# Optimization experiments

Measured on AMD Instinct MI355X. Metric: run time of the kernel, lower is better.

Reference implementation:

```python
import jax, jax.numpy as jnp
import numpy as np

B, T, I, H, O = 32, 2048, 128, 512, 128
FORGET_BIAS = 1.0


def setup_inputs() -> dict:
    key = jax.random.key(0)
    ks = jax.random.split(key, 8)
    s_ih = 1.0 / np.sqrt(H)
    data = jax.random.normal(ks[0], (B, T, I), dtype=jnp.float32)
    h0 = jnp.zeros((B, H), dtype=jnp.float32)
    c0 = jnp.zeros((B, H), dtype=jnp.float32)
    W_ih = jax.random.uniform(ks[1], (4 * H, I), minval=-s_ih, maxval=s_ih, dtype=jnp.float32)
    W_hh = jax.random.uniform(ks[2], (4 * H, H), minval=-s_ih, maxval=s_ih, dtype=jnp.float32)
    b_ih = jax.random.uniform(ks[3], (4 * H,), minval=-s_ih, maxval=s_ih, dtype=jnp.float32)
    b_hh = jax.random.uniform(ks[4], (4 * H,), minval=-s_ih, maxval=s_ih, dtype=jnp.float32)
    # forget-gate bias init: slice [H:2H] of each bias filled with forget_bias/2
    b_ih = b_ih.at[H:2 * H].set(FORGET_BIAS / 2)
    b_hh = b_hh.at[H:2 * H].set(FORGET_BIAS / 2)
    lin_W = jax.random.uniform(ks[5], (O, H), minval=-s_ih, maxval=s_ih, dtype=jnp.float32)
    lin_b = jax.random.uniform(ks[6], (O,), minval=-s_ih, maxval=s_ih, dtype=jnp.float32)
    return dict(data=data, h0=h0, c0=c0, W_ih=W_ih, W_hh=W_hh,
                b_ih=b_ih, b_hh=b_hh, lin_W=lin_W, lin_b=lin_b)


def reference(data, h0, c0, W_ih, W_hh, b_ih, b_hh, lin_W, lin_b):
    # LSTMCell loop over time (batch_first). PyTorch gate order: i, f, g, o.
    # Original code appends the CELL state (variable `hidden` = c) to hs and
    # decodes from the stacked cell states — reproduced faithfully.
    bias = b_ih + b_hh  # [4H]

    def step(carry, x_t):
        h, c = carry
        gates = x_t @ W_ih.T + h @ W_hh.T + bias  # [B, 4H]
        i_g, f_g, g_g, o_g = jnp.split(gates, 4, axis=-1)
        c_new = jax.nn.sigmoid(f_g) * c + jax.nn.sigmoid(i_g) * jnp.tanh(g_g)
        h_new = jax.nn.sigmoid(o_g) * jnp.tanh(c_new)
        return (h_new, c_new), c_new

    xs = jnp.swapaxes(data, 0, 1)  # [T, B, I]
    (h_f, c_f), cs = jax.lax.scan(step, (h0, c0), xs)
    output = jnp.swapaxes(cs, 0, 1)  # [B, T, H]
    decoded = output @ lin_W.T + lin_b  # [B, T, O]
    return decoded, h_f, c_f
```

## Files before the change

### kernel.cpp

```cpp
#include <hip/hip_runtime.h>
#include <hip/hip_bf16.h>


#define B_ 32
#define T_ 2048
#define I_ 128
#define H_ 512
#define O_ 128
#define NG 8
#define BPG 4
#define WPG 32
#define NWG 256
#define NTHR 512

#define HXS 648
#define CPS 520

typedef short bf16x8 __attribute__((ext_vector_type(8)));
typedef float f32x4 __attribute__((ext_vector_type(4)));
typedef unsigned long long u64;

static __device__ __forceinline__ unsigned f2bf(float f) {
  unsigned u = __float_as_uint(f);
  u = u + 0x7FFFu + ((u >> 16) & 1u);
  return u >> 16;
}
static __device__ __forceinline__ float bf2f(unsigned h) {
  return __uint_as_float(h << 16);
}
static __device__ __forceinline__ float fsigm(float x) {
  return 1.0f / (1.0f + __expf(-x));
}
static __device__ __forceinline__ float ftanh(float x) {
  return 1.0f - 2.0f / (__expf(2.0f * x) + 1.0f);
}

#define ALD(p) __hip_atomic_load((p), __ATOMIC_RELAXED, __HIP_MEMORY_SCOPE_AGENT)
#define AST(p, v) __hip_atomic_store((p), (v), __ATOMIC_RELAXED, __HIP_MEMORY_SCOPE_AGENT)

__global__ __launch_bounds__(NTHR, 2) void lstm_fused(
    const float* __restrict__ data, const float* __restrict__ h0,
    const float* __restrict__ c0, const float* __restrict__ W_ih,
    const float* __restrict__ W_hh, const float* __restrict__ b_ih,
    const float* __restrict__ b_hh, const float* __restrict__ lin_W,
    const float* __restrict__ lin_b, float* __restrict__ out,
    float* __restrict__ ws) {
  __shared__ alignas(16) unsigned short sHxHi[BPG * HXS];
  __shared__ alignas(16) unsigned short sHxLo[BPG * HXS];
  __shared__ alignas(16) float sCprev[BPG * CPS];
  __shared__ alignas(16) float sLinW[4 * CPS];
  __shared__ alignas(16) float sGates[2 * 64 * 4];
  __shared__ alignas(16) float sCst[64];
  __shared__ alignas(16) float sBias[64];
  __shared__ float sLinB[4];

  const int bid = blockIdx.x;
  const int g = bid & 7;
  const int wgi = bid >> 3;
  const int b0 = g * BPG;
  const int ubase = wgi * 16;
  const int tid = threadIdx.x;
  const int lane = tid & 63;
  const int w = tid >> 6;
  const int gate = w >> 1;
  const int kh = w & 1;
  const int m16 = lane & 15;
  const int kcg = lane >> 4;

  float* cb = ws;
  unsigned* hbPk = (unsigned*)(ws + 32768);
  int* cnt = (int*)(ws + 65536);

  bf16x8 fAhi[10], fAlo[10];
  const int grow = gate * H_ + ubase + m16;
#pragma unroll
  for (int kk = 0; kk < 10; kk++) {
    int k = kh * 320 + kk * 32 + kcg * 8;
    const float* src = (k < H_) ? (W_hh + (size_t)grow * H_ + k)
                                : (W_ih + (size_t)grow * I_ + (k - H_));
    float4 v0 = *(const float4*)src;
    float4 v1 = *(const float4*)(src + 4);
    float w8[8] = {v0.x, v0.y, v0.z, v0.w, v1.x, v1.y, v1.z, v1.w};
    union { unsigned short u[8]; bf16x8 v; } hi, lo;
#pragma unroll
    for (int j = 0; j < 8; j++) {
      unsigned h = f2bf(w8[j]);
      hi.u[j] = (unsigned short)h;
      lo.u[j] = (unsigned short)f2bf(w8[j] - bf2f(h));
    }
    fAhi[kk] = hi.v;
    fAlo[kk] = lo.v;
  }
  if (tid < 64) {
    int u_ = tid >> 2, ga = tid & 3;
    int r = ga * H_ + ubase + u_;
    sBias[u_ * 4 + ga] = b_ih[r] + b_hh[r];
  }
  if (tid >= 64 && tid < 128) {
    int q = tid - 64;
    sCst[q] = c0[(size_t)(b0 + (q & 3)) * H_ + ubase + (q >> 2)];
  }
  for (int idx = tid; idx < 4 * H_; idx += NTHR) {
    int o = idx >> 9, k = idx & (H_ - 1);
    sLinW[o * CPS + k] = lin_W[(size_t)(wgi * 4 + o) * H_ + k];
  }
  if (tid < 4) sLinB[tid] = lin_b[wgi * 4 + tid];

  if (tid < 256) {
    int b = tid >> 6, off = (tid & 63) * 8;
    const float* src = h0 + (size_t)(b0 + b) * H_ + off;
    float4 v0 = *(const float4*)src;
    float4 v1 = *(const float4*)(src + 4);
    float w8[8] = {v0.x, v0.y, v0.z, v0.w, v1.x, v1.y, v1.z, v1.w};
    union { unsigned short u[8]; uint4 q; } hi, lo;
#pragma unroll
    for (int j = 0; j < 8; j++) {
      unsigned h = f2bf(w8[j]);
      hi.u[j] = (unsigned short)h;
      lo.u[j] = (unsigned short)f2bf(w8[j] - bf2f(h));
    }
    *(uint4*)&sHxHi[b * HXS + off] = hi.q;
    *(uint4*)&sHxLo[b * HXS + off] = lo.q;
  }
  if (tid >= 256 && tid < 384) {
    int i = tid - 256, b = i >> 5, c4 = i & 31;
    float4 v = *(const float4*)(data + ((size_t)(b0 + b) * T_) * I_ + c4 * 4);
    float w4[4] = {v.x, v.y, v.z, v.w};
    union { unsigned short u[4]; uint2 q; } hi, lo;
#pragma unroll
    for (int j = 0; j < 4; j++) {
      unsigned h = f2bf(w4[j]);
      hi.u[j] = (unsigned short)h;
      lo.u[j] = (unsigned short)f2bf(w4[j] - bf2f(h));
    }
    *(uint2*)&sHxHi[b * HXS + H_ + c4 * 4] = hi.q;
    *(uint2*)&sHxLo[b * HXS + H_ + c4 * 4] = lo.q;
  }
  float4 pfx;
  if (tid >= 320 && tid < 448) {
    int i = tid - 320, b = i >> 5, c4 = i & 31;
    int tp = (T_ > 1) ? 1 : 0;
    pfx = *(const float4*)(data + ((size_t)(b0 + b) * T_ + tp) * I_ + c4 * 4);
  }
  __syncthreads();

  const int bcl = (m16 < BPG) ? m16 : (BPG - 1);
  const unsigned short* pBhi = sHxHi + bcl * HXS + kh * 320 + kcg * 8;
  const unsigned short* pBlo = sHxLo + bcl * HXS + kh * 320 + kcg * 8;

  for (int t = 0; t < T_; t++) {
    f32x4 a0 = {0.f, 0.f, 0.f, 0.f}, a1 = a0, a2 = a0;
#pragma unroll
    for (int kk = 0; kk < 10; kk++) {
      bf16x8 bh = *(const bf16x8*)(pBhi + kk * 32);
      bf16x8 bl = *(const bf16x8*)(pBlo + kk * 32);
      a0 = __builtin_amdgcn_mfma_f32_16x16x32_bf16(fAhi[kk], bh, a0, 0, 0, 0);
      a1 = __builtin_amdgcn_mfma_f32_16x16x32_bf16(fAhi[kk], bl, a1, 0, 0, 0);
      a2 = __builtin_amdgcn_mfma_f32_16x16x32_bf16(fAlo[kk], bh, a2, 0, 0, 0);
    }
    if (m16 < BPG) {
#pragma unroll
      for (int j = 0; j < 4; j++) {
        int up = kcg * 4 + j;
        sGates[(kh * 64 + up * 4 + m16) * 4 + gate] = a0[j] + a1[j] + a2[j];
      }
    }
    __syncthreads();

    if (tid < 64) {
      int up = tid >> 2, b = tid & 3;
      const float4 p0 = *(const float4*)&sGates[(up * 4 + b) * 4];
      const float4 p1 = *(const float4*)&sGates[(64 + up * 4 + b) * 4];
      float gi = p0.x + p1.x + sBias[up * 4 + 0];
      float gf = p0.y + p1.y + sBias[up * 4 + 1];
      float gg = p0.z + p1.z + sBias[up * 4 + 2];
      float go = p0.w + p1.w + sBias[up * 4 + 3];
      float cn = fsigm(gf) * sCst[tid] + fsigm(gi) * ftanh(gg);
      float hn = fsigm(go) * ftanh(cn);
      sCst[tid] = cn;
      size_t sbase = (((size_t)(t & 1) * NG + g) * BPG + b) * H_ + ubase + up;
      AST(&cb[sbase], cn);
      unsigned hh = f2bf(hn);
      unsigned hl = f2bf(hn - bf2f(hh));
      AST(&hbPk[sbase], (hh << 16) | hl);
      if (t == T_ - 1) {
        const size_t DEC = (size_t)B_ * T_ * O_;
        out[DEC + (size_t)(b0 + b) * H_ + ubase + up] = hn;
        out[DEC + (size_t)B_ * H_ + (size_t)(b0 + b) * H_ + ubase + up] = cn;
      }
      asm volatile("s_waitcnt vmcnt(0)" ::: "memory");
      if (tid == 0)
        __hip_atomic_fetch_add(&cnt[g * 16], 1, __ATOMIC_RELAXED,
                               __HIP_MEMORY_SCOPE_AGENT);
      const int target = WPG * (t + 1);
      while (ALD(&cnt[g * 16]) < target) {}
    } else if (tid < 320) {
      if (t > 0) {
        int q = (tid >> 4) - 4;
        int ks = tid & 15;
        int o = q >> 2, b = q & 3;
        float s = 0.f;
#pragma unroll
        for (int j = 0; j < 32; j++) {
          int k = ks + j * 16;
          s += sLinW[o * CPS + k] * sCprev[b * CPS + k];
        }
        s += __shfl_xor(s, 1);
        s += __shfl_xor(s, 2);
        s += __shfl_xor(s, 4);
        s += __shfl_xor(s, 8);
        if (ks == 0)
          out[((size_t)(b0 + b) * T_ + (t - 1)) * O_ + wgi * 4 + o] =
              s + sLinB[o];
      }
    } else if (tid < 448) {
      int i = tid - 320, b = i >> 5, c4 = i & 31;
      union { unsigned short u[4]; uint2 q; } hi, lo;
      float w4[4] = {pfx.x, pfx.y, pfx.z, pfx.w};
#pragma unroll
      for (int j = 0; j < 4; j++) {
        unsigned h = f2bf(w4[j]);
        hi.u[j] = (unsigned short)h;
        lo.u[j] = (unsigned short)f2bf(w4[j] - bf2f(h));
      }
      *(uint2*)&sHxHi[b * HXS + H_ + c4 * 4] = hi.q;
      *(uint2*)&sHxLo[b * HXS + H_ + c4 * 4] = lo.q;
      int tp = (t + 2 < T_) ? t + 2 : T_ - 1;
      pfx = *(const float4*)(data + ((size_t)(b0 + b) * T_ + tp) * I_ + c4 * 4);
    }
    __syncthreads();

    {
      int b = tid >> 7, u4 = (tid & 127) * 4;
      const size_t hbase = (((size_t)(t & 1) * NG + g) * BPG + b) * H_ + u4;
      u64 q0 = ALD((u64*)&hbPk[hbase]);
      u64 q1 = ALD((u64*)&hbPk[hbase + 2]);
      unsigned v0 = (unsigned)q0, v1 = (unsigned)(q0 >> 32);
      unsigned v2 = (unsigned)q1, v3 = (unsigned)(q1 >> 32);
      uint2 hw = {(v0 >> 16) | (v1 & 0xFFFF0000u),
                  (v2 >> 16) | (v3 & 0xFFFF0000u)};
      uint2 lw = {(v0 & 0xFFFFu) | ((v1 & 0xFFFFu) << 16),
                  (v2 & 0xFFFFu) | ((v3 & 0xFFFFu) << 16)};
      *(uint2*)&sHxHi[b * HXS + u4] = hw;
      *(uint2*)&sHxLo[b * HXS + u4] = lw;
      u64 c0q = ALD((u64*)&cb[hbase]);
      u64 c1q = ALD((u64*)&cb[hbase + 2]);
      float4 cf = {__uint_as_float((unsigned)c0q),
                   __uint_as_float((unsigned)(c0q >> 32)),
                   __uint_as_float((unsigned)c1q),
                   __uint_as_float((unsigned)(c1q >> 32))};
      *(float4*)&sCprev[b * CPS + u4] = cf;
    }
    __syncthreads();
  }

  {
    int q = tid >> 5, ks = tid & 31, o = q >> 2, b = q & 3;
    float s = 0.f;
#pragma unroll
    for (int j = 0; j < 16; j++) {
      int k = ks + j * 32;
      s += sLinW[o * CPS + k] * sCprev[b * CPS + k];
    }
    s += __shfl_xor(s, 1);
    s += __shfl_xor(s, 2);
    s += __shfl_xor(s, 4);
    s += __shfl_xor(s, 8);
    s += __shfl_xor(s, 16);
    if (ks == 0)
      out[((size_t)(b0 + b) * T_ + (T_ - 1)) * O_ + wgi * 4 + o] =
          s + sLinB[o];
  }
}

extern "C" void kernel_launch(void* const* d_in, const int* in_sizes, int n_in,
                              void* d_out, int out_size, void* d_ws, size_t ws_size,
                              hipStream_t stream) {
  const float* data = (const float*)d_in[0];
  const float* h0 = (const float*)d_in[1];
  const float* c0 = (const float*)d_in[2];
  const float* W_ih = (const float*)d_in[3];
  const float* W_hh = (const float*)d_in[4];
  const float* b_ih = (const float*)d_in[5];
  const float* b_hh = (const float*)d_in[6];
  const float* lin_W = (const float*)d_in[7];
  const float* lin_b = (const float*)d_in[8];
  float* out = (float*)d_out;
  float* ws = (float*)d_ws;

  hipMemsetAsync((char*)d_ws + 65536 * 4, 0, NG * 16 * sizeof(int), stream);

  hipLaunchKernelGGL(lstm_fused, dim3(NWG), dim3(NTHR), 0, stream, data, h0, c0,
                     W_ih, W_hh, b_ih, b_hh, lin_W, lin_b, out, ws);
}
```

Measured before the change: 6.012 ms.

## Replace per-step counter barrier with canary-flagged packed h/c mailbox exchange

Each step's cross-workgroup sync via an atomic counter spin is replaced by a 4-deep ring of 64-bit slots, each packing the fp32 cell state with the bf16 hi/lo hidden state. Readers spin until no slot holds the canary value, and spare threads re-poison the slot from two steps earlier. Bias and cell state move into registers, the cell buffer is double-buffered, and one block barrier per step becomes a lighter s_barrier. This removes the counter round trip and the split h/c loads, but relies on the canary never matching real data and on relaxed-ordering visibility of the payload.

```diff
diff --git a/kernel.cpp b/kernel.cpp
--- a/kernel.cpp
+++ b/kernel.cpp
@@ -12,9 +12,11 @@
 #define WPG 32
 #define NWG 256
 #define NTHR 512
-
-#define HXS 648
+#define NBUF 4
+
+#define HXS 656
 #define CPS 520
+#define CAN 0xAAAAAAAAu
 
 typedef short bf16x8 __attribute__((ext_vector_type(8)));
 typedef float f32x4 __attribute__((ext_vector_type(4)));
@@ -37,6 +39,7 @@
 
 #define ALD(p) __hip_atomic_load((p), __ATOMIC_RELAXED, __HIP_MEMORY_SCOPE_AGENT)
 #define AST(p, v) __hip_atomic_store((p), (v), __ATOMIC_RELAXED, __HIP_MEMORY_SCOPE_AGENT)
+#define BARRIER() asm volatile("s_waitcnt lgkmcnt(0)\ns_barrier" ::: "memory")
 
 __global__ __launch_bounds__(NTHR, 2) void lstm_fused(
     const float* __restrict__ data, const float* __restrict__ h0,
@@ -47,11 +50,9 @@
     float* __restrict__ ws) {
   __shared__ alignas(16) unsigned short sHxHi[BPG * HXS];
   __shared__ alignas(16) unsigned short sHxLo[BPG * HXS];
-  __shared__ alignas(16) float sCprev[BPG * CPS];
+  __shared__ alignas(16) float sCp[2][BPG * CPS];
   __shared__ alignas(16) float sLinW[4 * CPS];
-  __shared__ alignas(16) float sGates[2 * 64 * 4];
-  __shared__ alignas(16) float sCst[64];
-  __shared__ alignas(16) float sBias[64];
+  __shared__ alignas(16) float sGates[4][2][68];
   __shared__ float sLinB[4];
 
   const int bid = blockIdx.x;
@@ -67,9 +68,8 @@
   const int m16 = lane & 15;
   const int kcg = lane >> 4;
 
-  float* cb = ws;
-  unsigned* hbPk = (unsigned*)(ws + 32768);
-  int* cnt = (int*)(ws + 65536);
+  u64* hcPk = (u64*)ws;
+  int* cnt = (int*)(ws + (size_t)NBUF * NG * BPG * H_ * 2);
 
   bf16x8 fAhi[10], fAlo[10];
   const int grow = gate * H_ + ubase + m16;
@@ -91,14 +91,15 @@
     fAhi[kk] = hi.v;
     fAlo[kk] = lo.v;
   }
+  float bias_[4], c_state = 0.f;
   if (tid < 64) {
-    int u_ = tid >> 2, ga = tid & 3;
-    int r = ga * H_ + ubase + u_;
-    sBias[u_ * 4 + ga] = b_ih[r] + b_hh[r];
-  }
-  if (tid >= 64 && tid < 128) {
-    int q = tid - 64;
-    sCst[q] = c0[(size_t)(b0 + (q & 3)) * H_ + ubase + (q >> 2)];
+    int up = tid >> 2, b = tid & 3;
+#pragma unroll
+    for (int ga = 0; ga < 4; ga++) {
+      int r = ga * H_ + ubase + up;
+      bias_[ga] = b_ih[r] + b_hh[r];
+    }
+    c_state = c0[(size_t)(b0 + b) * H_ + ubase + up];
   }
   for (int idx = tid; idx < 4 * H_; idx += NTHR) {
     int o = idx >> 9, k = idx & (H_ - 1);
@@ -142,6 +143,19 @@
     int tp = (T_ > 1) ? 1 : 0;
     pfx = *(const float4*)(data + ((size_t)(b0 + b) * T_ + tp) * I_ + c4 * 4);
   }
+  if (tid < 256) {
+    int buf = tid >> 6, q = tid & 63, up = q >> 2, b = q & 3;
+    AST(&hcPk[(((size_t)buf * NG + g) * BPG + b) * H_ + ubase + up],
+        0xAAAAAAAAAAAAAAAAull);
+  }
+  asm volatile("s_waitcnt vmcnt(0)" ::: "memory");
+  __syncthreads();
+  if (tid == 0)
+    __hip_atomic_fetch_add(&cnt[g * 16], 1, __ATOMIC_RELAXED,
+                           __HIP_MEMORY_SCOPE_AGENT);
+  if (tid < 64) {
+    while (ALD(&cnt[g * 16]) < WPG) {}
+  }
   __syncthreads();
 
   const int bcl = (m16 < BPG) ? m16 : (BPG - 1);
@@ -161,49 +175,40 @@
     if (m16 < BPG) {
 #pragma unroll
       for (int j = 0; j < 4; j++) {
-        int up = kcg * 4 + j;
-        sGates[(kh * 64 + up * 4 + m16) * 4 + gate] = a0[j] + a1[j] + a2[j];
-      }
-    }
-    __syncthreads();
+        sGates[gate][kh][kcg * 16 + j * 4 + m16] = a0[j] + a1[j] + a2[j];
+      }
+    }
+    BARRIER();
 
     if (tid < 64) {
       int up = tid >> 2, b = tid & 3;
-      const float4 p0 = *(const float4*)&sGates[(up * 4 + b) * 4];
-      const float4 p1 = *(const float4*)&sGates[(64 + up * 4 + b) * 4];
-      float gi = p0.x + p1.x + sBias[up * 4 + 0];
-      float gf = p0.y + p1.y + sBias[up * 4 + 1];
-      float gg = p0.z + p1.z + sBias[up * 4 + 2];
-      float go = p0.w + p1.w + sBias[up * 4 + 3];
-      float cn = fsigm(gf) * sCst[tid] + fsigm(gi) * ftanh(gg);
+      float gi = sGates[0][0][tid] + sGates[0][1][tid] + bias_[0];
+      float gf = sGates[1][0][tid] + sGates[1][1][tid] + bias_[1];
+      float gg = sGates[2][0][tid] + sGates[2][1][tid] + bias_[2];
+      float go = sGates[3][0][tid] + sGates[3][1][tid] + bias_[3];
+      float cn = fsigm(gf) * c_state + fsigm(gi) * ftanh(gg);
       float hn = fsigm(go) * ftanh(cn);
-      sCst[tid] = cn;
-      size_t sbase = (((size_t)(t & 1) * NG + g) * BPG + b) * H_ + ubase + up;
-      AST(&cb[sbase], cn);
+      c_state = cn;
       unsigned hh = f2bf(hn);
       unsigned hl = f2bf(hn - bf2f(hh));
-      AST(&hbPk[sbase], (hh << 16) | hl);
+      u64 pay = ((u64)__float_as_uint(cn) << 32) | (u64)((hh << 16) | hl);
+      AST(&hcPk[(((size_t)(t & 3) * NG + g) * BPG + b) * H_ + ubase + up], pay);
       if (t == T_ - 1) {
         const size_t DEC = (size_t)B_ * T_ * O_;
         out[DEC + (size_t)(b0 + b) * H_ + ubase + up] = hn;
         out[DEC + (size_t)B_ * H_ + (size_t)(b0 + b) * H_ + ubase + up] = cn;
       }
-      asm volatile("s_waitcnt vmcnt(0)" ::: "memory");
-      if (tid == 0)
-        __hip_atomic_fetch_add(&cnt[g * 16], 1, __ATOMIC_RELAXED,
-                               __HIP_MEMORY_SCOPE_AGENT);
-      const int target = WPG * (t + 1);
-      while (ALD(&cnt[g * 16]) < target) {}
     } else if (tid < 320) {
       if (t > 0) {
         int q = (tid >> 4) - 4;
         int ks = tid & 15;
         int o = q >> 2, b = q & 3;
+        const float* cp = sCp[(t & 1) ^ 1];
         float s = 0.f;
 #pragma unroll
         for (int j = 0; j < 32; j++) {
           int k = ks + j * 16;
-          s += sLinW[o * CPS + k] * sCprev[b * CPS + k];
+          s += sLinW[o * CPS + k] * cp[b * CPS + k];
         }
         s += __shfl_xor(s, 1);
         s += __shfl_xor(s, 2);
@@ -227,40 +232,55 @@
       *(uint2*)&sHxLo[b * HXS + H_ + c4 * 4] = lo.q;
       int tp = (t + 2 < T_) ? t + 2 : T_ - 1;
       pfx = *(const float4*)(data + ((size_t)(b0 + b) * T_ + tp) * I_ + c4 * 4);
-    }
-    __syncthreads();
+    } else {
+      if (t >= 2) {
+        int q = tid - 448, up7 = q >> 2, b7 = q & 3;
+        AST(&hcPk[(((size_t)((t - 2) & 3) * NG + g) * BPG + b7) * H_ + ubase +
+                  up7],
+            0xAAAAAAAAAAAAAAAAull);
+        asm volatile("s_waitcnt vmcnt(0)" ::: "memory");
+      }
+    }
 
     {
       int b = tid >> 7, u4 = (tid & 127) * 4;
-      const size_t hbase = (((size_t)(t & 1) * NG + g) * BPG + b) * H_ + u4;
-      u64 q0 = ALD((u64*)&hbPk[hbase]);
-      u64 q1 = ALD((u64*)&hbPk[hbase + 2]);
-      unsigned v0 = (unsigned)q0, v1 = (unsigned)(q0 >> 32);
-      unsigned v2 = (unsigned)q1, v3 = (unsigned)(q1 >> 32);
-      uint2 hw = {(v0 >> 16) | (v1 & 0xFFFF0000u),
-                  (v2 >> 16) | (v3 & 0xFFFF0000u)};
-      uint2 lw = {(v0 & 0xFFFFu) | ((v1 & 0xFFFFu) << 16),
-                  (v2 & 0xFFFFu) | ((v3 & 0xFFFFu) << 16)};
+      const u64* sp =
+          hcPk + (((size_t)(t & 3) * NG + g) * BPG + b) * H_ + u4;
+      u64 v0, v1, v2, v3;
+      for (;;) {
+        v0 = ALD(sp);
+        v1 = ALD(sp + 1);
+        v2 = ALD(sp + 2);
+        v3 = ALD(sp + 3);
+        if (((unsigned)v0 != CAN) & ((unsigned)v1 != CAN) &
+            ((unsigned)v2 != CAN) & ((unsigned)v3 != CAN))
+          break;
+      }
+      unsigned p0 = (unsigned)v0, p1 = (unsigned)v1, p2 = (unsigned)v2,
+               p3 = (unsigned)v3;
+      uint2 hw = {(p0 >> 16) | (p1 & 0xFFFF0000u),
+                  (p2 >> 16) | (p3 & 0xFFFF0000u)};
+      uint2 lw = {(p0 & 0xFFFFu) | (p1 << 16),
+                  (p2 & 0xFFFFu) | (p3 << 16)};
       *(uint2*)&sHxHi[b * HXS + u4] = hw;
       *(uint2*)&sHxLo[b * HXS + u4] = lw;
-      u64 c0q = ALD((u64*)&cb[hbase]);
-      u64 c1q = ALD((u64*)&cb[hbase + 2]);
-      float4 cf = {__uint_as_float((unsigned)c0q),
-                   __uint_as_float((unsigned)(c0q >> 32)),
-                   __uint_as_float((unsigned)c1q),
-                   __uint_as_float((unsigned)(c1q >> 32))};
-      *(float4*)&sCprev[b * CPS + u4] = cf;
-    }
-    __syncthreads();
+      float4 cf = {__uint_as_float((unsigned)(v0 >> 32)),
+                   __uint_as_float((unsigned)(v1 >> 32)),
+                   __uint_as_float((unsigned)(v2 >> 32)),
+                   __uint_as_float((unsigned)(v3 >> 32))};
+      *(float4*)&sCp[t & 1][b * CPS + u4] = cf;
+    }
+    BARRIER();
   }
 
   {
     int q = tid >> 5, ks = tid & 31, o = q >> 2, b = q & 3;
+    const float* cp = sCp[(T_ - 1) & 1];
     float s = 0.f;
 #pragma unroll
     for (int j = 0; j < 16; j++) {
       int k = ks + j * 32;
-      s += sLinW[o * CPS + k] * sCprev[b * CPS + k];
+      s += sLinW[o * CPS + k] * cp[b * CPS + k];
     }
     s += __shfl_xor(s, 1);
     s += __shfl_xor(s, 2);
@@ -288,7 +308,8 @@
   float* out = (float*)d_out;
   float* ws = (float*)d_ws;
 
-  hipMemsetAsync((char*)d_ws + 65536 * 4, 0, NG * 16 * sizeof(int), stream);
+  const size_t CNT_OFF = (size_t)NBUF * NG * BPG * H_ * 8;
+  hipMemsetAsync((char*)d_ws + CNT_OFF, 0, NG * 16 * sizeof(int), stream);
 
   hipLaunchKernelGGL(lstm_fused, dim3(NWG), dim3(NTHR), 0, stream, data, h0, c0,
                      W_ih, W_hh, b_ih, b_hh, lin_W, lin_b, out, ws);
```

Result: faster. 5.505 ms (-8.4%).
